# Optimization experiments

Hardware: AMD Instinct MI355X
Metric: run time of the kernel (lower is better)

The kernel has to match this reference:

```python
import jax, jax.numpy as jnp
import numpy as np

BS = 1024        # BATCH_SIZE
IA = 3           # INPUT_AXIS
A = BS * IA      # 3072
D = BS * (IA - 1)  # 2048


def _linear(x, w, b):
    # torch Linear: y = x @ W^T + b, W is [out, in]
    return x @ w.T + b


def _pdist_flat(a):
    # a: [BS, d] -> flat [BS*BS] pairwise Euclidean distances.
    # The original adds min(a) to both coords; it cancels in the difference.
    d2 = jnp.sum((a[:, None, :] - a[None, :, :]) ** 2, axis=-1)  # [BS, BS]
    return jnp.sqrt(d2).reshape(-1)


def setup_inputs() -> dict:
    key = jax.random.key(0)
    ks = jax.random.split(key, 17)
    s = 0.02
    inp = {"x": jax.random.normal(ks[0], (A,), dtype=jnp.float32)}
    # encoder: Linear(A,A), Linear(A,A), Linear(A,A), Linear(A,D)
    enc_shapes = [(A, A), (A, A), (A, A), (D, A)]
    # decoder: Linear(D,A), Linear(A,A), Linear(A,A), Linear(A,A)
    dec_shapes = [(A, D), (A, A), (A, A), (A, A)]
    i = 1
    for j, (o, n) in enumerate(enc_shapes, 1):
        inp[f"ew{j}"] = jax.random.normal(ks[i], (o, n), dtype=jnp.float32) * s; i += 1
        inp[f"eb{j}"] = jnp.zeros((o,), dtype=jnp.float32)
    for j, (o, n) in enumerate(dec_shapes, 1):
        inp[f"dw{j}"] = jax.random.normal(ks[i], (o, n), dtype=jnp.float32) * s; i += 1
        inp[f"db{j}"] = jnp.zeros((o,), dtype=jnp.float32)
    return inp


def reference(x, ew1, eb1, ew2, eb2, ew3, eb3, ew4, eb4,
              dw1, db1, dw2, db2, dw3, db3, dw4, db4):
    # encoder: Lin+Tanh, Lin+Tanh, Lin, Lin, Tanhshrink
    h = jnp.tanh(_linear(x, ew1, eb1))
    h = jnp.tanh(_linear(h, ew2, eb2))
    h = _linear(h, ew3, eb3)
    h = _linear(h, ew4, eb4)
    y = h - jnp.tanh(h)  # Tanhshrink, shape [D]

    in_data = x.reshape(BS, IA)
    lat_repr = y.reshape(BS, IA - 1)

    in_diff_sum = jax.lax.stop_gradient(_pdist_flat(in_data))    # [BS*BS]
    lat_diff_sum = jax.lax.stop_gradient(_pdist_flat(lat_repr))  # [BS*BS]

    # decoder: Lin+Tanh, Lin+Tanh, Lin, Lin, Tanh
    g = jnp.tanh(_linear(y, dw1, db1))
    g = jnp.tanh(_linear(g, dw2, db2))
    g = _linear(g, dw3, db3)
    g = _linear(g, dw4, db4)
    output = jnp.tanh(g)  # [A]

    return (output, in_diff_sum, lat_diff_sum, lat_repr)
```

## Files before the change

kernel.cpp:

```cpp
#include <hip/hip_runtime.h>
#include <math.h>

#define BS 1024
#define AA 3072
#define DD 2048
#define PDBLK (BS * BS / 256)

template<int IN_DIM, int ACT, int PD, int NROW>
__global__ __launch_bounds__(256, 8) void matvec_pd(
    const float* __restrict__ W, const float* __restrict__ b,
    const float* __restrict__ x, float* __restrict__ y,
    float* __restrict__ y2, float* __restrict__ pd_out)
{
    const int t = (int)threadIdx.x;

    if ((int)blockIdx.x >= NROW) {
        if (PD != 0) {
            int idx = (((int)blockIdx.x - NROW) << 8) | t;
            int i = idx >> 10, j = idx & 1023;
            if (PD == 3) {
                float d0 = x[3 * i + 0] - x[3 * j + 0];
                float d1 = x[3 * i + 1] - x[3 * j + 1];
                float d2 = x[3 * i + 2] - x[3 * j + 2];
                pd_out[idx] = sqrtf(d0 * d0 + d1 * d1 + d2 * d2);
            } else {
                float d0 = x[2 * i + 0] - x[2 * j + 0];
                float d1 = x[2 * i + 1] - x[2 * j + 1];
                pd_out[idx] = sqrtf(d0 * d0 + d1 * d1);
            }
        }
        return;
    }

    const int row = (int)blockIdx.x;
    const float4* __restrict__ Wr = (const float4*)(W + (size_t)row * IN_DIM);
    const float4* __restrict__ xv = (const float4*)x;

    constexpr int N4 = IN_DIM / 4;
    float sum = 0.f;
#pragma unroll
    for (int it = 0; it < N4 / 256; ++it) {
        int i = t + it * 256;
        float4 w4 = Wr[i];
        float4 x4 = xv[i];
        sum += w4.x * x4.x + w4.y * x4.y + w4.z * x4.z + w4.w * x4.w;
    }

#pragma unroll
    for (int off = 32; off; off >>= 1) sum += __shfl_down(sum, off);

    __shared__ float part[4];
    if ((t & 63) == 0) part[t >> 6] = sum;
    __syncthreads();
    if (t == 0) {
        float v = part[0] + part[1] + part[2] + part[3] + b[row];
        if (ACT == 1)      v = tanhf(v);
        else if (ACT == 2) v = v - tanhf(v);
        y[row] = v;
        if (y2) y2[row] = v;
    }
}

extern "C" void kernel_launch(void* const* d_in, const int* in_sizes, int n_in,
                              void* d_out, int out_size, void* d_ws, size_t ws_size,
                              hipStream_t stream)
{
    const float* x   = (const float*)d_in[0];
    const float* ew1 = (const float*)d_in[1];  const float* eb1 = (const float*)d_in[2];
    const float* ew2 = (const float*)d_in[3];  const float* eb2 = (const float*)d_in[4];
    const float* ew3 = (const float*)d_in[5];  const float* eb3 = (const float*)d_in[6];
    const float* ew4 = (const float*)d_in[7];  const float* eb4 = (const float*)d_in[8];
    const float* dw1 = (const float*)d_in[9];  const float* db1 = (const float*)d_in[10];
    const float* dw2 = (const float*)d_in[11]; const float* db2 = (const float*)d_in[12];
    const float* dw3 = (const float*)d_in[13]; const float* db3 = (const float*)d_in[14];
    const float* dw4 = (const float*)d_in[15]; const float* db4 = (const float*)d_in[16];

    float* out      = (float*)d_out;
    float* out_y    = out;
    float* out_ind  = out + AA;
    float* out_lat  = out_ind + BS * BS;
    float* out_rep  = out_lat + BS * BS;

    float* ws = (float*)d_ws;
    float* h1 = ws;
    float* h2 = h1 + AA;
    float* h3 = h2 + AA;
    float* yy = h3 + AA;
    float* g1 = yy + DD;
    float* g2 = g1 + AA;
    float* g3 = g2 + AA;

    dim3 blk(256);

    matvec_pd<AA, 1, 3, AA><<<AA + PDBLK, blk, 0, stream>>>(ew1, eb1, x,  h1, nullptr, out_ind);
    matvec_pd<AA, 1, 0, AA><<<AA,         blk, 0, stream>>>(ew2, eb2, h1, h2, nullptr, nullptr);
    matvec_pd<AA, 0, 0, AA><<<AA,         blk, 0, stream>>>(ew3, eb3, h2, h3, nullptr, nullptr);
    matvec_pd<AA, 2, 0, DD><<<DD,         blk, 0, stream>>>(ew4, eb4, h3, yy, out_rep, nullptr);

    matvec_pd<DD, 1, 2, AA><<<AA + PDBLK, blk, 0, stream>>>(dw1, db1, yy, g1, nullptr, out_lat);
    matvec_pd<AA, 1, 0, AA><<<AA,         blk, 0, stream>>>(dw2, db2, g1, g2, nullptr, nullptr);
    matvec_pd<AA, 0, 0, AA><<<AA,         blk, 0, stream>>>(dw3, db3, g2, g3, nullptr, nullptr);
    matvec_pd<AA, 1, 0, AA><<<AA,         blk, 0, stream>>>(dw4, db4, g3, out_y, nullptr, nullptr);
}
```

Baseline: 286.2 us.

## Prefetch next layer weights into cache with extra blocks in each matvec

Each matvec launch gets extra blocks that read the next layer's weight matrix and discard the result, to warm the large last-level cache (Infinity Cache) while the current layer computes. The aim is for the next kernel's weight reads to hit cache instead of HBM. The cost is that the current kernel does more memory traffic and competes with its own weight reads. Each weight matrix is 24-36MB, so it may not stay resident, and there is a risk the prefetch evicts the current layer's data.

```diff
diff --git a/kernel.cpp b/kernel.cpp
--- a/kernel.cpp
+++ b/kernel.cpp
@@ -5,14 +5,30 @@
 #define AA 3072
 #define DD 2048
 #define PDBLK (BS * BS / 256)
+#define PFBLK 384
 
-template<int IN_DIM, int ACT, int PD, int NROW>
+template<int IN_DIM, int ACT, int PD, int NROW, int PFN4>
 __global__ __launch_bounds__(256, 8) void matvec_pd(
     const float* __restrict__ W, const float* __restrict__ b,
     const float* __restrict__ x, float* __restrict__ y,
-    float* __restrict__ y2, float* __restrict__ pd_out)
+    float* __restrict__ y2, float* __restrict__ pd_out,
+    const float4* __restrict__ Wnext)
 {
     const int t = (int)threadIdx.x;
+    constexpr int PDB = (PD != 0) ? PDBLK : 0;
+
+    if ((int)blockIdx.x >= NROW + PDB) {
+        if (PFN4 > 0) {
+            float acc = 0.f;
+            for (long i = (long)((int)blockIdx.x - NROW - PDB) * 256 + t;
+                 i < (long)PFN4; i += (long)PFBLK * 256) {
+                float4 v = Wnext[i];
+                acc += v.x + v.y + v.z + v.w;
+            }
+            asm volatile("" :: "v"(acc));
+        }
+        return;
+    }
 
     if ((int)blockIdx.x >= NROW) {
         if (PD != 0) {
@@ -90,15 +106,26 @@
     float* g2 = g1 + AA;
     float* g3 = g2 + AA;
 
+    constexpr int N4_AA = AA * AA / 4;
+    constexpr int N4_AD = AA * DD / 4;
+
     dim3 blk(256);
 
-    matvec_pd<AA, 1, 3, AA><<<AA + PDBLK, blk, 0, stream>>>(ew1, eb1, x,  h1, nullptr, out_ind);
-    matvec_pd<AA, 1, 0, AA><<<AA,         blk, 0, stream>>>(ew2, eb2, h1, h2, nullptr, nullptr);
-    matvec_pd<AA, 0, 0, AA><<<AA,         blk, 0, stream>>>(ew3, eb3, h2, h3, nullptr, nullptr);
-    matvec_pd<AA, 2, 0, DD><<<DD,         blk, 0, stream>>>(ew4, eb4, h3, yy, out_rep, nullptr);
+    matvec_pd<AA, 1, 3, AA, N4_AA><<<AA + PDBLK + PFBLK, blk, 0, stream>>>(
+        ew1, eb1, x,  h1, nullptr, out_ind, (const float4*)ew2);
+    matvec_pd<AA, 1, 0, AA, N4_AA><<<AA + PFBLK, blk, 0, stream>>>(
+        ew2, eb2, h1, h2, nullptr, nullptr, (const float4*)ew3);
+    matvec_pd<AA, 0, 0, AA, N4_AD><<<AA + PFBLK, blk, 0, stream>>>(
+        ew3, eb3, h2, h3, nullptr, nullptr, (const float4*)ew4);
+    matvec_pd<AA, 2, 0, DD, N4_AD><<<DD + PFBLK, blk, 0, stream>>>(
+        ew4, eb4, h3, yy, out_rep, nullptr, (const float4*)dw1);
 
-    matvec_pd<DD, 1, 2, AA><<<AA + PDBLK, blk, 0, stream>>>(dw1, db1, yy, g1, nullptr, out_lat);
-    matvec_pd<AA, 1, 0, AA><<<AA,         blk, 0, stream>>>(dw2, db2, g1, g2, nullptr, nullptr);
-    matvec_pd<AA, 0, 0, AA><<<AA,         blk, 0, stream>>>(dw3, db3, g2, g3, nullptr, nullptr);
-    matvec_pd<AA, 1, 0, AA><<<AA,         blk, 0, stream>>>(dw4, db4, g3, out_y, nullptr, nullptr);
+    matvec_pd<DD, 1, 2, AA, N4_AA><<<AA + PDBLK + PFBLK, blk, 0, stream>>>(
+        dw1, db1, yy, g1, nullptr, out_lat, (const float4*)dw2);
+    matvec_pd<AA, 1, 0, AA, N4_AA><<<AA + PFBLK, blk, 0, stream>>>(
+        dw2, db2, g1, g2, nullptr, nullptr, (const float4*)dw3);
+    matvec_pd<AA, 0, 0, AA, N4_AA><<<AA + PFBLK, blk, 0, stream>>>(
+        dw3, db3, g2, g3, nullptr, nullptr, (const float4*)dw4);
+    matvec_pd<AA, 1, 0, AA, 0><<<AA, blk, 0, stream>>>(
+        dw4, db4, g3, out_y, nullptr, nullptr, nullptr);
 }
```

New measurement: 337.6 us. 18.0% more time.
